# Optimization experiments

Measured on AMD Instinct MI355X. Metric: run time of the kernel, lower is better.

Reference implementation:

```python
import jax, jax.numpy as jnp
from jax import lax
import numpy as np

B, T, I, H, C = 32, 256, 128, 128, 100


def setup_inputs() -> dict:
    key = jax.random.key(0)
    ks = jax.random.split(key, 9)
    s = 1.0 / np.sqrt(H)  # PyTorch LSTMCell init range
    inp = {
        "x": jax.random.normal(ks[0], (B, T, I), dtype=jnp.float32),
        "w_ih": jax.random.uniform(ks[1], (4 * H, I), jnp.float32, -s, s),
        "b_ih": jax.random.uniform(ks[2], (4 * H,), jnp.float32, -s, s),
        "w_hh": jax.random.uniform(ks[3], (4 * H, H), jnp.float32, -s, s),
        "b_hh": jax.random.uniform(ks[4], (4 * H,), jnp.float32, -s, s),
        # attention params: normal(mean=0, std=0.01) per the source
        "w1": 0.01 * jax.random.normal(ks[5], (2 * H, H), dtype=jnp.float32),
        "w2": 0.01 * jax.random.normal(ks[6], (H, 1), dtype=jnp.float32),
        "w_fc": jax.random.uniform(ks[7], (C, H), jnp.float32, -s, s),
        "b_fc": jax.random.uniform(ks[8], (C,), jnp.float32, -s, s),
    }
    return inp


def _forward(x, w_ih, b_ih, w_hh, b_hh, w1, w2, w_fc, b_fc):
    Bv, Tv, _ = x.shape
    Hv = w_hh.shape[1]
    h0 = jnp.zeros((Bv, Hv), x.dtype)
    c0 = jnp.zeros((Bv, Hv), x.dtype)
    # memory buffer: slot 0 holds the initial zero hidden state (as in the
    # torch code, h_old starts as h_t=0); slots 1..T filled as we go.
    # Unwritten (future) slots are zero, so their attn contribution
    # attn_w * h_old is exactly zero -> no mask needed, matching the
    # growing-memory semantics of the original loop.
    mem0 = jnp.zeros((Bv, Tv + 1, Hv), x.dtype)
    attn0 = jnp.zeros((Bv, Hv), x.dtype)

    def step(carry, inp):
        h, c, mem, _ = carry
        x_t, i = inp
        # PyTorch LSTMCell: gate order i, f, g, o
        gates = x_t @ w_ih.T + b_ih + h @ w_hh.T + b_hh
        ig, fg, gg, og = jnp.split(gates, 4, axis=-1)
        c = jax.nn.sigmoid(fg) * c + jax.nn.sigmoid(ig) * jnp.tanh(gg)
        h = jax.nn.sigmoid(og) * jnp.tanh(c)
        # additive attention scores over the memory (NO softmax in source)
        h_rep = jnp.broadcast_to(h[:, None, :], mem.shape)  # [B, T+1, H]
        cat = jnp.concatenate([h_rep, mem], axis=-1)        # [B, T+1, 2H]
        s = jnp.tanh(cat @ w1) @ w2                          # [B, T+1, 1]
        attn_c = jnp.sum(s * mem, axis=1)                    # [B, H]
        mem = mem.at[:, i + 1, :].set(h)  # append h_t to memory
        return (h, c, mem, attn_c), None

    xs = (jnp.transpose(x, (1, 0, 2)), jnp.arange(Tv))
    (h, c, mem, attn_c), _ = lax.scan(step, (h0, c0, mem0, attn0), xs)
    return (h + attn_c) @ w_fc.T + b_fc


def reference(x, w_ih, b_ih, w_hh, b_hh, w1, w2, w_fc, b_fc):
    return _forward(x, w_ih, b_ih, w_hh, b_hh, w1, w2, w_fc, b_fc)
```

## Files before the change

kernel.cpp:

```cpp
#include <hip/hip_runtime.h>
#include <hip/hip_bf16.h>


#define Bsz 32
#define Tsz 256
#define Isz 128
#define Hsz 128
#define Csz 100
#define G4H 512

typedef short v8s __attribute__((ext_vector_type(8)));
typedef float v4fa __attribute__((ext_vector_type(4)));

__device__ __forceinline__ float2 pk_fma(float2 a, float2 b, float2 c) {
    float2 d;
    asm("v_pk_fma_f32 %0, %1, %2, %3" : "=v"(d) : "v"(a), "v"(b), "v"(c));
    return d;
}
__device__ __forceinline__ float quad_rsum(float x) {
    int t = __builtin_amdgcn_update_dpp(0, __float_as_int(x), 0xB1, 0xF, 0xF, true);
    x += __int_as_float(t);
    t = __builtin_amdgcn_update_dpp(0, __float_as_int(x), 0x4E, 0xF, 0xF, true);
    x += __int_as_float(t);
    return x;
}
__device__ __forceinline__ float rcpf(float x) { return __builtin_amdgcn_rcpf(x); }
__device__ __forceinline__ float sigm_n(float x) { return rcpf(1.0f + __expf(-x)); }
__device__ __forceinline__ float tanh_n(float x) {
    float ax = fabsf(x);
    float e = __expf(-2.0f * ax);
    float t = (1.0f - e) * rcpf(1.0f + e);
    return copysignf(t, x);
}
__device__ __forceinline__ float tanh_s(float x) { return tanh_n(x); }
__device__ __forceinline__ short bf16_bits(float x) {
    __hip_bfloat16 h = __float2bfloat16(x);
    return *reinterpret_cast<short*>(&h);
}
__device__ __forceinline__ float bf16_val(float x) {
    return __bfloat162float(__float2bfloat16(x));
}

__global__ __launch_bounds__(256) void prep_kernel(
    const float* __restrict__ w_ih, const float* __restrict__ b_ih,
    const float* __restrict__ w_hh, const float* __restrict__ b_hh,
    const float* __restrict__ w1,
    __hip_bfloat16* __restrict__ W2ih, __hip_bfloat16* __restrict__ W2v,
    float* __restrict__ whh_pk, float* __restrict__ bias,
    float* __restrict__ attn_c) {
    int idx = blockIdx.x * blockDim.x + threadIdx.x;
    if (idx < G4H * Isz) {
        int n = idx >> 7;
        int k = idx & 127;
        float x = w_ih[idx];
        __hip_bfloat16 hi = __float2bfloat16(x);
        __hip_bfloat16 lo = __float2bfloat16(x - __bfloat162float(hi));
        W2ih[(size_t)n * 384 + k] = hi;
        W2ih[(size_t)n * 384 + 128 + k] = lo;
        W2ih[(size_t)n * 384 + 256 + k] = hi;

        int j4  = idx & 3;
        int q   = (idx >> 2) & 3;
        int d   = (idx >> 4) & 127;
        int gi  = (idx >> 11) & 3;
        int kk4 = (idx >> 13) & 7;
        whh_pk[idx] = w_hh[(size_t)((gi << 7) + d) * 128 + (q << 5) + (kk4 << 2) + j4];
    }
    if (idx < Hsz * Hsz) {
        int n = idx >> 7;
        int k = idx & 127;
        float x = w1[(size_t)(128 + k) * Hsz + n];
        __hip_bfloat16 hi = __float2bfloat16(x);
        __hip_bfloat16 lo = __float2bfloat16(x - __bfloat162float(hi));
        W2v[(size_t)n * 384 + k] = hi;
        W2v[(size_t)n * 384 + 128 + k] = lo;
        W2v[(size_t)n * 384 + 256 + k] = hi;
    }
    if (idx < G4H) bias[idx] = b_ih[idx] + b_hh[idx];
    if (idx < Bsz * Hsz) attn_c[idx] = 0.0f;
}

__global__ __launch_bounds__(256) void gemm_mfma_f32a(
    const float* __restrict__ A, const __hip_bfloat16* __restrict__ W2,
    const float* __restrict__ bias, float* __restrict__ C, int M, int N) {
    const int tid = threadIdx.x;
    const int w = tid >> 6, lane = tid & 63;
    const int m0 = blockIdx.y * 64 + (w & 1) * 32;
    const int n0 = blockIdx.x * 64 + (w >> 1) * 32;
    const int r = lane & 15, quad = lane >> 4;

    v8s Ahi[2][4], Alo[2][4];
    #pragma unroll
    for (int i = 0; i < 2; ++i)
        #pragma unroll
        for (int cb = 0; cb < 4; ++cb) {
            const float* src = A + (size_t)(m0 + 16 * i + r) * Isz + cb * 32 + quad * 8;
            float4 f0 = *(const float4*)src;
            float4 f1 = *(const float4*)(src + 4);
            float f[8] = {f0.x, f0.y, f0.z, f0.w, f1.x, f1.y, f1.z, f1.w};
            v8s hi, lo;
            #pragma unroll
            for (int e = 0; e < 8; ++e) {
                float hv = bf16_val(f[e]);
                hi[e] = bf16_bits(f[e]);
                lo[e] = bf16_bits(f[e] - hv);
            }
            Ahi[i][cb] = hi;
            Alo[i][cb] = lo;
        }

    v4fa acc[2][2] = {};
    const short* Wb = (const short*)W2;
    #pragma unroll
    for (int ks = 0; ks < 12; ++ks) {
        int cb = ks & 3;
        v8s a0 = (ks >= 8) ? Alo[0][cb] : Ahi[0][cb];
        v8s a1 = (ks >= 8) ? Alo[1][cb] : Ahi[1][cb];
        int kb = ks * 32 + quad * 8;
        v8s b0 = *(const v8s*)(Wb + (size_t)(n0 + r) * 384 + kb);
        v8s b1 = *(const v8s*)(Wb + (size_t)(n0 + 16 + r) * 384 + kb);
        acc[0][0] = __builtin_amdgcn_mfma_f32_16x16x32_bf16(a0, b0, acc[0][0], 0, 0, 0);
        acc[0][1] = __builtin_amdgcn_mfma_f32_16x16x32_bf16(a0, b1, acc[0][1], 0, 0, 0);
        acc[1][0] = __builtin_amdgcn_mfma_f32_16x16x32_bf16(a1, b0, acc[1][0], 0, 0, 0);
        acc[1][1] = __builtin_amdgcn_mfma_f32_16x16x32_bf16(a1, b1, acc[1][1], 0, 0, 0);
    }
    #pragma unroll
    for (int i = 0; i < 2; ++i)
        #pragma unroll
        for (int j = 0; j < 2; ++j) {
            int cn = n0 + 16 * j + r;
            float bb = bias ? bias[cn] : 0.0f;
            #pragma unroll
            for (int rr = 0; rr < 4; ++rr) {
                int row = m0 + 16 * i + quad * 4 + rr;
                C[(size_t)row * N + cn] = acc[i][j][rr] + bb;
            }
        }
}

#define HPAD(k) ((k) + 8 * ((k) >> 5))

__global__ __launch_bounds__(512, 2) void lstm_seq(
    const float* __restrict__ G, const float* __restrict__ whh_pk,
    float* __restrict__ H_all) {
    const int b = blockIdx.x;
    const int tid = threadIdx.x;
    const int d = tid >> 2;
    const int q = tid & 3;

    __shared__ float h_s[2][160];

    float2 w2v[4][16];
    {
        const float4* wp = (const float4*)whh_pk;
        #pragma unroll
        for (int kk4 = 0; kk4 < 8; ++kk4)
            #pragma unroll
            for (int gi = 0; gi < 4; ++gi) {
                float4 v = wp[((kk4 * 4 + gi) * 128 + d) * 4 + q];
                w2v[gi][kk4 * 2]     = make_float2(v.x, v.y);
                w2v[gi][kk4 * 2 + 1] = make_float2(v.z, v.w);
            }
    }

    if (tid < 320) ((float*)h_s)[tid] = 0.0f;
    float c = 0.0f;
    __syncthreads();

    const float* Gq = G + (size_t)b * Tsz * G4H + q * 128 + d;
    float* Hst = H_all + (size_t)b * Tsz * Hsz + d;

    float gval = Gq[0];
    int cur = 0;
    for (int t = 0; t < Tsz; ++t) {
        const int tn = (t < Tsz - 1) ? t + 1 : t;
        float ngval = Gq[(size_t)tn * G4H];

        float2 accA[4], accB[4];
        #pragma unroll
        for (int gi = 0; gi < 4; ++gi) {
            accA[gi] = make_float2(q == gi ? gval : 0.f, 0.f);
            accB[gi] = make_float2(0.f, 0.f);
        }
        const float4* hb4 = (const float4*)&h_s[cur][q * 40];
        #pragma unroll
        for (int kk4 = 0; kk4 < 8; ++kk4) {
            float4 h4 = hb4[kk4];
            float2 hA = make_float2(h4.x, h4.y);
            float2 hB = make_float2(h4.z, h4.w);
            accA[0] = pk_fma(hA, w2v[0][2 * kk4], accA[0]);
            accA[1] = pk_fma(hA, w2v[1][2 * kk4], accA[1]);
            accA[2] = pk_fma(hA, w2v[2][2 * kk4], accA[2]);
            accA[3] = pk_fma(hA, w2v[3][2 * kk4], accA[3]);
            accB[0] = pk_fma(hB, w2v[0][2 * kk4 + 1], accB[0]);
            accB[1] = pk_fma(hB, w2v[1][2 * kk4 + 1], accB[1]);
            accB[2] = pk_fma(hB, w2v[2][2 * kk4 + 1], accB[2]);
            accB[3] = pk_fma(hB, w2v[3][2 * kk4 + 1], accB[3]);
        }
        float a0 = quad_rsum(accA[0].x + accA[0].y + accB[0].x + accB[0].y);
        float a1 = quad_rsum(accA[1].x + accA[1].y + accB[1].x + accB[1].y);
        float a2 = quad_rsum(accA[2].x + accA[2].y + accB[2].x + accB[2].y);
        float a3 = quad_rsum(accA[3].x + accA[3].y + accB[3].x + accB[3].y);

        float iv = sigm_n(a0);
        float fv = sigm_n(a1);
        float gv = tanh_n(a2);
        float ov = sigm_n(a3);
        c = fv * c + iv * gv;
        float h = ov * tanh_n(c);

        if (q == 0) {
            h_s[cur ^ 1][HPAD(d)] = h;
            Hst[(size_t)t * Hsz] = h;
        }
        gval = ngval;
        __syncthreads();
        cur ^= 1;
    }
}

__global__ __launch_bounds__(256) void scores_part(
    const float* __restrict__ H_all, const float* __restrict__ KV,
    const float* __restrict__ w1, const float* __restrict__ w2,
    float* __restrict__ attn_c) {
    const int b = blockIdx.y, jt = blockIdx.x;
    const int tid = threadIdx.x;
    __shared__ float hT[Hsz];
    __shared__ float q_s[Hsz];
    __shared__ float w2s[Hsz];
    __shared__ float s_s[64];
    __shared__ float part[2][Hsz];

    const float* Hb = H_all + (size_t)b * Tsz * Hsz;
    const float* KVb = KV + (size_t)b * Tsz * Hsz;

    if (tid < Hsz) {
        hT[tid] = Hb[255 * Hsz + tid];
        w2s[tid] = w2[tid];
    }
    __syncthreads();
    if (tid < Hsz) {
        float acc = 0.f;
        #pragma unroll 8
        for (int k = 0; k < Hsz; ++k) acc = fmaf(hT[k], w1[k * Hsz + tid], acc);
        q_s[tid] = acc;
    }
    __syncthreads();

    const int jl = tid >> 2, ql = tid & 3;
    const int j = jt * 64 + jl;
    float p = 0.f;
    if (j < 255) {
        const float* kv = KVb + (size_t)j * Hsz + ql * 32;
        const float* qs = q_s + ql * 32;
        const float* wv = w2s + ql * 32;
        #pragma unroll 8
        for (int k = 0; k < 32; ++k)
            p = fmaf(tanh_s(qs[k] + kv[k]), wv[k], p);
    }
    p = quad_rsum(p);
    if (ql == 0) s_s[jl] = (j < 255) ? p : 0.0f;
    __syncthreads();

    {
        const int dd = tid & 127, half = tid >> 7;
        float acc = 0.f;
        #pragma unroll 4
        for (int u = 0; u < 32; ++u) {
            int lj = half * 32 + u;
            int jj = jt * 64 + lj;
            if (jj < 255) acc = fmaf(s_s[lj], Hb[(size_t)jj * Hsz + dd], acc);
        }
        part[half][dd] = acc;
    }
    __syncthreads();
    if (tid < Hsz) atomicAdd(&attn_c[b * Hsz + tid], part[0][tid] + part[1][tid]);
}

__global__ __launch_bounds__(256) void fc_out(
    const float* __restrict__ H_all, const float* __restrict__ attn_c,
    const float* __restrict__ w_fc, const float* __restrict__ b_fc,
    float* __restrict__ out) {
    const int b = blockIdx.x, tid = threadIdx.x;
    __shared__ float r_s[Hsz];
    if (tid < Hsz)
        r_s[tid] = H_all[(size_t)b * Tsz * Hsz + 255 * Hsz + tid] + attn_c[b * Hsz + tid];
    __syncthreads();
    const int o = tid >> 1, half = tid & 1;
    float acc = 0.f;
    if (o < Csz) {
        const float* wr = w_fc + (size_t)o * Hsz + half * 64;
        const float* rr = r_s + half * 64;
        #pragma unroll 8
        for (int k = 0; k < 64; ++k) acc = fmaf(rr[k], wr[k], acc);
    }
    acc += __shfl_xor(acc, 1);
    if (half == 0 && o < Csz) out[b * Csz + o] = acc + b_fc[o];
}

extern "C" void kernel_launch(void* const* d_in, const int* in_sizes, int n_in,
                              void* d_out, int out_size, void* d_ws, size_t ws_size,
                              hipStream_t stream) {
    const float* x    = (const float*)d_in[0];
    const float* w_ih = (const float*)d_in[1];
    const float* b_ih = (const float*)d_in[2];
    const float* w_hh = (const float*)d_in[3];
    const float* b_hh = (const float*)d_in[4];
    const float* w1   = (const float*)d_in[5];
    const float* w2   = (const float*)d_in[6];
    const float* w_fc = (const float*)d_in[7];
    const float* b_fc = (const float*)d_in[8];

    float* ws = (float*)d_ws;
    float* whh_pk = ws;
    float* bias   = whh_pk + 65536;
    float* attn_c = bias + 512;
    __hip_bfloat16* W2ih = (__hip_bfloat16*)(attn_c + 4096);
    __hip_bfloat16* W2v  = (__hip_bfloat16*)(attn_c + 4096 + 98304);
    float* G      = attn_c + 4096 + 98304 + 24576;
    float* H_all  = G + 4194304;
    float* KV     = H_all + 1048576;

    prep_kernel<<<256, 256, 0, stream>>>(w_ih, b_ih, w_hh, b_hh, w1,
                                         W2ih, W2v, whh_pk, bias, attn_c);

    dim3 gG(G4H / 64, (Bsz * Tsz) / 64);
    gemm_mfma_f32a<<<gG, 256, 0, stream>>>(x, W2ih, bias, G, Bsz * Tsz, G4H);

    lstm_seq<<<Bsz, 512, 0, stream>>>(G, whh_pk, H_all);

    dim3 gK(Hsz / 64, (Bsz * Tsz) / 64);
    gemm_mfma_f32a<<<gK, 256, 0, stream>>>(H_all, W2v, nullptr, KV, Bsz * Tsz, Hsz);

    dim3 gS(4, Bsz);
    scores_part<<<gS, 256, 0, stream>>>(H_all, KV, w1, w2, attn_c);

    fc_out<<<Bsz, 256, 0, stream>>>(H_all, attn_c, w_fc, b_fc, (float*)d_out);
}
```

Before: 329.6 us.

## Fuse attention scores with final FC and streamline LSTM activations

Merges scores_part and fc_out into one per-batch kernel, which removes the attn_c atomics, its zeroing in prep, and one kernel launch. Rewrites sigmoid and tanh with exp2 plus reciprocal in a branch-free form, which shortens the serial per-step critical path of the LSTM recurrence. Hoists the shared-memory h loads ahead of the FMA loop and changes the launch attribute to amdgpu_waves_per_eu. The fused attention kernel runs only 32 blocks, so its parallelism drops, and the new tanh form may lose accuracy for small inputs.

```diff
diff --git a/kernel.cpp b/kernel.cpp
--- a/kernel.cpp
+++ b/kernel.cpp
@@ -25,14 +25,13 @@
     return x;
 }
 __device__ __forceinline__ float rcpf(float x) { return __builtin_amdgcn_rcpf(x); }
-__device__ __forceinline__ float sigm_n(float x) { return rcpf(1.0f + __expf(-x)); }
+__device__ __forceinline__ float ex2(float x) { return __builtin_amdgcn_exp2f(x); }
+__device__ __forceinline__ float sigm_n(float x) {
+    return rcpf(1.0f + ex2(-1.442695041f * x));
+}
 __device__ __forceinline__ float tanh_n(float x) {
-    float ax = fabsf(x);
-    float e = __expf(-2.0f * ax);
-    float t = (1.0f - e) * rcpf(1.0f + e);
-    return copysignf(t, x);
-}
-__device__ __forceinline__ float tanh_s(float x) { return tanh_n(x); }
+    return fmaf(-2.0f, rcpf(1.0f + ex2(2.885390082f * x)), 1.0f);
+}
 __device__ __forceinline__ short bf16_bits(float x) {
     __hip_bfloat16 h = __float2bfloat16(x);
     return *reinterpret_cast<short*>(&h);
@@ -46,8 +45,7 @@
     const float* __restrict__ w_hh, const float* __restrict__ b_hh,
     const float* __restrict__ w1,
     __hip_bfloat16* __restrict__ W2ih, __hip_bfloat16* __restrict__ W2v,
-    float* __restrict__ whh_pk, float* __restrict__ bias,
-    float* __restrict__ attn_c) {
+    float* __restrict__ whh_pk, float* __restrict__ bias) {
     int idx = blockIdx.x * blockDim.x + threadIdx.x;
     if (idx < G4H * Isz) {
         int n = idx >> 7;
@@ -77,7 +75,6 @@
         W2v[(size_t)n * 384 + 256 + k] = hi;
     }
     if (idx < G4H) bias[idx] = b_ih[idx] + b_hh[idx];
-    if (idx < Bsz * Hsz) attn_c[idx] = 0.0f;
 }
 
 __global__ __launch_bounds__(256) void gemm_mfma_f32a(
@@ -140,7 +137,9 @@
 
 #define HPAD(k) ((k) + 8 * ((k) >> 5))
 
-__global__ __launch_bounds__(512, 2) void lstm_seq(
+__global__ __launch_bounds__(512)
+__attribute__((amdgpu_waves_per_eu(2, 2)))
+void lstm_seq(
     const float* __restrict__ G, const float* __restrict__ whh_pk,
     float* __restrict__ H_all) {
     const int b = blockIdx.x;
@@ -176,18 +175,21 @@
         const int tn = (t < Tsz - 1) ? t + 1 : t;
         float ngval = Gq[(size_t)tn * G4H];
 
+        const float4* hb4 = (const float4*)&h_s[cur][q * 40];
+        float4 h4[8];
+        #pragma unroll
+        for (int kk4 = 0; kk4 < 8; ++kk4) h4[kk4] = hb4[kk4];
+
         float2 accA[4], accB[4];
         #pragma unroll
         for (int gi = 0; gi < 4; ++gi) {
             accA[gi] = make_float2(q == gi ? gval : 0.f, 0.f);
             accB[gi] = make_float2(0.f, 0.f);
         }
-        const float4* hb4 = (const float4*)&h_s[cur][q * 40];
         #pragma unroll
         for (int kk4 = 0; kk4 < 8; ++kk4) {
-            float4 h4 = hb4[kk4];
-            float2 hA = make_float2(h4.x, h4.y);
-            float2 hB = make_float2(h4.z, h4.w);
+            float2 hA = make_float2(h4[kk4].x, h4[kk4].y);
+            float2 hB = make_float2(h4[kk4].z, h4[kk4].w);
             accA[0] = pk_fma(hA, w2v[0][2 * kk4], accA[0]);
             accA[1] = pk_fma(hA, w2v[1][2 * kk4], accA[1]);
             accA[2] = pk_fma(hA, w2v[2][2 * kk4], accA[2]);
@@ -197,16 +199,20 @@
             accB[2] = pk_fma(hB, w2v[2][2 * kk4 + 1], accB[2]);
             accB[3] = pk_fma(hB, w2v[3][2 * kk4 + 1], accB[3]);
         }
-        float a0 = quad_rsum(accA[0].x + accA[0].y + accB[0].x + accB[0].y);
-        float a1 = quad_rsum(accA[1].x + accA[1].y + accB[1].x + accB[1].y);
-        float a2 = quad_rsum(accA[2].x + accA[2].y + accB[2].x + accB[2].y);
-        float a3 = quad_rsum(accA[3].x + accA[3].y + accB[3].x + accB[3].y);
+        float2 s0 = make_float2(accA[0].x + accB[0].x, accA[0].y + accB[0].y);
+        float2 s1 = make_float2(accA[1].x + accB[1].x, accA[1].y + accB[1].y);
+        float2 s2 = make_float2(accA[2].x + accB[2].x, accA[2].y + accB[2].y);
+        float2 s3 = make_float2(accA[3].x + accB[3].x, accA[3].y + accB[3].y);
+        float a0 = quad_rsum(s0.x + s0.y);
+        float a1 = quad_rsum(s1.x + s1.y);
+        float a2 = quad_rsum(s2.x + s2.y);
+        float a3 = quad_rsum(s3.x + s3.y);
 
         float iv = sigm_n(a0);
         float fv = sigm_n(a1);
         float gv = tanh_n(a2);
         float ov = sigm_n(a3);
-        c = fv * c + iv * gv;
+        c = fmaf(fv, c, iv * gv);
         float h = ov * tanh_n(c);
 
         if (q == 0) {
@@ -219,16 +225,17 @@
     }
 }
 
-__global__ __launch_bounds__(256) void scores_part(
+__global__ __launch_bounds__(256) void attn_fc(
     const float* __restrict__ H_all, const float* __restrict__ KV,
     const float* __restrict__ w1, const float* __restrict__ w2,
-    float* __restrict__ attn_c) {
-    const int b = blockIdx.y, jt = blockIdx.x;
+    const float* __restrict__ w_fc, const float* __restrict__ b_fc,
+    float* __restrict__ out) {
+    const int b = blockIdx.x;
     const int tid = threadIdx.x;
     __shared__ float hT[Hsz];
     __shared__ float q_s[Hsz];
     __shared__ float w2s[Hsz];
-    __shared__ float s_s[64];
+    __shared__ float s_s[256];
     __shared__ float part[2][Hsz];
 
     const float* Hb = H_all + (size_t)b * Tsz * Hsz;
@@ -248,54 +255,47 @@
     __syncthreads();
 
     const int jl = tid >> 2, ql = tid & 3;
-    const int j = jt * 64 + jl;
-    float p = 0.f;
-    if (j < 255) {
-        const float* kv = KVb + (size_t)j * Hsz + ql * 32;
-        const float* qs = q_s + ql * 32;
-        const float* wv = w2s + ql * 32;
-        #pragma unroll 8
-        for (int k = 0; k < 32; ++k)
-            p = fmaf(tanh_s(qs[k] + kv[k]), wv[k], p);
-    }
-    p = quad_rsum(p);
-    if (ql == 0) s_s[jl] = (j < 255) ? p : 0.0f;
+    #pragma unroll
+    for (int it = 0; it < 4; ++it) {
+        const int j = it * 64 + jl;
+        float p = 0.f;
+        if (j < 255) {
+            const float* kv = KVb + (size_t)j * Hsz + ql * 32;
+            const float* qs = q_s + ql * 32;
+            const float* wv = w2s + ql * 32;
+            #pragma unroll 8
+            for (int k = 0; k < 32; ++k)
+                p = fmaf(tanh_n(qs[k] + kv[k]), wv[k], p);
+        }
+        p = quad_rsum(p);
+        if (ql == 0) s_s[j] = (j < 255) ? p : 0.0f;
+    }
     __syncthreads();
 
     {
         const int dd = tid & 127, half = tid >> 7;
         float acc = 0.f;
         #pragma unroll 4
-        for (int u = 0; u < 32; ++u) {
-            int lj = half * 32 + u;
-            int jj = jt * 64 + lj;
-            if (jj < 255) acc = fmaf(s_s[lj], Hb[(size_t)jj * Hsz + dd], acc);
+        for (int u = 0; u < 128; ++u) {
+            int jj = half * 128 + u;
+            if (jj < 255) acc = fmaf(s_s[jj], Hb[(size_t)jj * Hsz + dd], acc);
         }
         part[half][dd] = acc;
     }
     __syncthreads();
-    if (tid < Hsz) atomicAdd(&attn_c[b * Hsz + tid], part[0][tid] + part[1][tid]);
-}
-
-__global__ __launch_bounds__(256) void fc_out(
-    const float* __restrict__ H_all, const float* __restrict__ attn_c,
-    const float* __restrict__ w_fc, const float* __restrict__ b_fc,
-    float* __restrict__ out) {
-    const int b = blockIdx.x, tid = threadIdx.x;
-    __shared__ float r_s[Hsz];
-    if (tid < Hsz)
-        r_s[tid] = H_all[(size_t)b * Tsz * Hsz + 255 * Hsz + tid] + attn_c[b * Hsz + tid];
-    __syncthreads();
-    const int o = tid >> 1, half = tid & 1;
+    if (tid < Hsz) q_s[tid] = hT[tid] + part[0][tid] + part[1][tid];
+    __syncthreads();
+
+    const int o = tid >> 1, hf = tid & 1;
     float acc = 0.f;
     if (o < Csz) {
-        const float* wr = w_fc + (size_t)o * Hsz + half * 64;
-        const float* rr = r_s + half * 64;
+        const float* wr = w_fc + (size_t)o * Hsz + hf * 64;
+        const float* rr = q_s + hf * 64;
         #pragma unroll 8
         for (int k = 0; k < 64; ++k) acc = fmaf(rr[k], wr[k], acc);
     }
     acc += __shfl_xor(acc, 1);
-    if (half == 0 && o < Csz) out[b * Csz + o] = acc + b_fc[o];
+    if (hf == 0 && o < Csz) out[b * Csz + o] = acc + b_fc[o];
 }
 
 extern "C" void kernel_launch(void* const* d_in, const int* in_sizes, int n_in,
@@ -314,15 +314,14 @@
     float* ws = (float*)d_ws;
     float* whh_pk = ws;
     float* bias   = whh_pk + 65536;
-    float* attn_c = bias + 512;
-    __hip_bfloat16* W2ih = (__hip_bfloat16*)(attn_c + 4096);
-    __hip_bfloat16* W2v  = (__hip_bfloat16*)(attn_c + 4096 + 98304);
-    float* G      = attn_c + 4096 + 98304 + 24576;
+    __hip_bfloat16* W2ih = (__hip_bfloat16*)(bias + 512);
+    __hip_bfloat16* W2v  = (__hip_bfloat16*)(bias + 512 + 98304);
+    float* G      = bias + 512 + 98304 + 24576;
     float* H_all  = G + 4194304;
     float* KV     = H_all + 1048576;
 
     prep_kernel<<<256, 256, 0, stream>>>(w_ih, b_ih, w_hh, b_hh, w1,
-                                         W2ih, W2v, whh_pk, bias, attn_c);
+                                         W2ih, W2v, whh_pk, bias);
 
     dim3 gG(G4H / 64, (Bsz * Tsz) / 64);
     gemm_mfma_f32a<<<gG, 256, 0, stream>>>(x, W2ih, bias, G, Bsz * Tsz, G4H);
@@ -332,8 +331,5 @@
     dim3 gK(Hsz / 64, (Bsz * Tsz) / 64);
     gemm_mfma_f32a<<<gK, 256, 0, stream>>>(H_all, W2v, nullptr, KV, Bsz * Tsz, Hsz);
 
-    dim3 gS(4, Bsz);
-    scores_part<<<gS, 256, 0, stream>>>(H_all, KV, w1, w2, attn_c);
-
-    fc_out<<<Bsz, 256, 0, stream>>>(H_all, attn_c, w_fc, b_fc, (float*)d_out);
-}
+    attn_fc<<<Bsz, 256, 0, stream>>>(H_all, KV, w1, w2, w_fc, b_fc, (float*)d_out);
+}
```

New measurement: 389.8 us. 1.18x slower.
